# Optimization experiments

Measured on AMD Instinct MI355X. Metric: run time of the kernel, lower is better.

The kernel has to match this reference:

```python
import jax, jax.numpy as jnp
import numpy as np

B = 2
SEQ = 384            # args.seq_len (per-stock sub-sequence length)
N_AUX = 4            # len(args.aux_tickers)
S = SEQ * N_AUX + 1  # global separator token + tiled sub-sequences
D_MODEL = 512
NHEAD = 8
HEAD_DIM = 64
ROPE = 32            # qk_rope_dim
KV_C = 256
Q_C = 384
D_FF = 1536
H2 = NHEAD * 2       # differential attention sub-heads
DH = HEAD_DIM // 2
RH = ROPE // 2
EPS = 1.1920929e-07  # torch RMSNorm default eps (fp32 machine eps)
SCALING = 1.0 / ((HEAD_DIM + ROPE) // 2)
LAMBDA_INIT = 0.8 - 0.6 * float(np.exp(-0.3 * 0))  # depth=0 -> 0.2


def rmsnorm(x, w, eps=EPS):
    return x * jax.lax.rsqrt(jnp.mean(jnp.square(x), -1, keepdims=True) + eps) * w


def apply_rope(xs, cos, sin):
    # xs: [B, N_AUX, SEQ, H2, RH]; cos/sin: [SEQ, RH//2]
    xr = xs[..., 0::2]
    xi = xs[..., 1::2]
    c = cos[None, None, :, None, :]
    s = sin[None, None, :, None, :]
    yr = xr * c - xi * s
    yi = xr * s + xi * c
    return jnp.stack([yr, yi], axis=-1).reshape(xs.shape)


def _build_mask():
    causal = np.triu(np.ones((SEQ, SEQ), np.bool_), 1)
    tiled = np.tile(causal, (N_AUX, N_AUX))
    m = np.ones((S, S), np.bool_)
    m[:, 0] = False          # everyone attends to global separator
    m[1:, 1:] = tiled
    return jnp.asarray(m)[None, None]  # [1,1,S,S], True = masked


MASK = _build_mask()


def setup_inputs() -> dict:
    key = jax.random.key(0)
    ks = jax.random.split(key, 16)

    def w(k, shape, std=0.02):
        return jax.random.normal(k, shape, jnp.float32) * std

    x = jax.random.normal(ks[0], (B, S, D_MODEL), jnp.float32)
    # rope table: complex [SEQ, ROPE//4] stored as (cos, sin)
    pairs = ROPE // 4
    inv = 1.0 / (10000.0 ** (np.arange(pairs, dtype=np.float64) / pairs))
    ang = np.outer(np.arange(SEQ), inv)
    freqs = jnp.asarray(np.stack([np.cos(ang), np.sin(ang)], -1), jnp.float32)
    return {
        'x': x,
        'freqs': freqs,
        'W_kv_down': w(ks[1], (D_MODEL, KV_C + ROPE)),
        'W_q_down': w(ks[2], (D_MODEL, Q_C)),
        'W_kv_up': w(ks[3], (KV_C, NHEAD * HEAD_DIM * 2)),
        'W_q_up': w(ks[4], (Q_C, NHEAD * (HEAD_DIM + ROPE))),
        'kv_norm_w': jnp.ones((KV_C,), jnp.float32),
        'q_norm_w': jnp.ones((Q_C,), jnp.float32),
        'W_o': w(ks[5], (NHEAD * HEAD_DIM, D_MODEL)),
        'lambda_q1': w(ks[6], (DH,), 0.1),
        'lambda_k1': w(ks[7], (DH,), 0.1),
        'lambda_q2': w(ks[8], (DH,), 0.1),
        'lambda_k2': w(ks[9], (DH,), 0.1),
        'head_norm_w': jnp.ones((HEAD_DIM,), jnp.float32),
        'norm1_w': jnp.ones((D_MODEL,), jnp.float32),
        'norm2_w': jnp.ones((D_MODEL,), jnp.float32),
        'W_ff_in': w(ks[10], (D_MODEL, 2 * D_FF)),
        'W_ff_out': w(ks[11], (D_FF, D_MODEL)),
    }


def reference(x, freqs, W_kv_down, W_q_down, W_kv_up, W_q_up, kv_norm_w, q_norm_w,
              W_o, lambda_q1, lambda_k1, lambda_q2, lambda_k2, head_norm_w,
              norm1_w, norm2_w, W_ff_in, W_ff_out):
    cos, sin = freqs[..., 0], freqs[..., 1]
    # ---- attention block (pre-norm) ----
    h = rmsnorm(x, norm1_w)
    ckv_full = h @ W_kv_down                               # [B,S,KV_C+ROPE]
    c_kv, k_rope = ckv_full[..., :KV_C], ckv_full[..., KV_C:]
    kv = (rmsnorm(c_kv, kv_norm_w) @ W_kv_up).reshape(B, S, NHEAD, 2 * HEAD_DIM)
    k, v = kv[..., :HEAD_DIM], kv[..., HEAD_DIM:]
    k = k.reshape(B, S, H2, DH)
    qf = (rmsnorm(h @ W_q_down, q_norm_w) @ W_q_up).reshape(B, S, NHEAD, HEAD_DIM + ROPE)
    q, q_rope = qf[..., :HEAD_DIM], qf[..., HEAD_DIM:]
    q = q.reshape(B, S, H2, DH)
    k_rope = jnp.broadcast_to(k_rope[:, :, None, :], (B, S, NHEAD, ROPE)).reshape(B, S, H2, RH)
    q_rope = q_rope.reshape(B, S, H2, RH)
    # split off global separator token, rope per sub-sequence
    q_sep, q_rot = q_rope[:, :1], q_rope[:, 1:].reshape(B, N_AUX, SEQ, H2, RH)
    k_sep, k_rot = k_rope[:, :1], k_rope[:, 1:].reshape(B, N_AUX, SEQ, H2, RH)
    q_rot = apply_rope(q_rot, cos, sin).reshape(B, S - 1, H2, RH)
    k_rot = apply_rope(k_rot, cos, sin).reshape(B, S - 1, H2, RH)
    q_rope = jnp.concatenate([q_sep, q_rot], axis=1)
    k_rope = jnp.concatenate([k_sep, k_rot], axis=1)
    qh = jnp.concatenate([q, q_rope], -1).transpose(0, 2, 1, 3)  # [B,H2,S,DH+RH]
    kh = jnp.concatenate([k, k_rope], -1).transpose(0, 2, 1, 3)
    a = jnp.einsum('bhqd,bhkd->bhqk', qh, kh) * SCALING
    abs_a = jnp.where(MASK, -1e9, jnp.abs(a))
    p = jnp.sign(a) * jax.nn.softmax(abs_a, axis=-1)
    lam = (jnp.exp(jnp.sum(lambda_q1 * lambda_k1)) -
           jnp.exp(jnp.sum(lambda_q2 * lambda_k2)) + LAMBDA_INIT)
    p = p.reshape(B, NHEAD, 2, S, S)
    G = jnp.mean(p[:, :, 0], axis=-1, keepdims=True)
    att = p[:, :, 0] - lam * p[:, :, 1] + G * lam
    att = jnp.where(MASK, 0.0, att)
    o = jnp.einsum('bhqk,bkhd->bqhd', att, v)              # [B,S,NHEAD,HEAD_DIM]
    o = rmsnorm(o, head_norm_w, 1e-5).reshape(B, S, NHEAD * HEAD_DIM)
    x = x + o @ W_o
    # ---- SwiGLU FFN ----
    h2 = rmsnorm(x, norm2_w)
    uv = h2 @ W_ff_in
    u, g = uv[..., :D_FF], uv[..., D_FF:]
    return x + (u * jax.nn.silu(g)) @ W_ff_out
```

## Files before the change

kernel.cpp:

```cpp
#include <hip/hip_runtime.h>

#define NB 2
#define SEQN 384
#define NS 1537
#define NS_PAD 1600
#define NH 8
#define H2N 16
#define NM (NB*NS)
#define DFF 1536
#define EPS1 1.1920929e-07f
#define SCAL (1.0f/48.0f)
#define SC2 (SCAL * 1.4426950408889634f)

#define SWZ(row, col) ((((row) << 6)) + ((col) ^ (((row) & 7) << 3)))

typedef __bf16 bf16x8 __attribute__((ext_vector_type(8)));
typedef _Float16 f16x8 __attribute__((ext_vector_type(8)));
typedef float f32x4 __attribute__((ext_vector_type(4)));

__device__ __forceinline__ unsigned short f2bf(float f) {
    unsigned int u = __builtin_bit_cast(unsigned int, f);
    u += 0x7FFFu + ((u >> 16) & 1u);
    return (unsigned short)(u >> 16);
}
__device__ __forceinline__ float bf2f(unsigned short h) {
    unsigned int u = ((unsigned int)h) << 16;
    return __builtin_bit_cast(float, u);
}

struct TD { const float* w; unsigned short* hi; unsigned short* lo; int K; int N; };
struct TD7 { TD d[7]; int tend[7]; };

__global__ __launch_bounds__(256) void transpose_all(TD7 a) {
    __shared__ float tile[32][33];
    int t = blockIdx.x;
    int i = 0;
    while (t >= a.tend[i]) i++;
    int base = (i == 0) ? 0 : a.tend[i - 1];
    int lt = t - base;
    const float* w = a.d[i].w;
    unsigned short* hi = a.d[i].hi;
    unsigned short* lo = a.d[i].lo;
    int K = a.d[i].K, N = a.d[i].N;
    int kt = (K + 31) / 32;
    int k0 = (lt % kt) * 32, n0 = (lt / kt) * 32;
    int tx = threadIdx.x & 31, ty4 = (threadIdx.x >> 5) * 4;
    for (int q = 0; q < 4; q++) {
        int k = k0 + ty4 + q, n = n0 + tx;
        tile[ty4 + q][tx] = (k < K && n < N) ? w[(size_t)k * N + n] : 0.f;
    }
    __syncthreads();
    for (int q = 0; q < 4; q++) {
        int n = n0 + ty4 + q, k = k0 + tx;
        if (n < N && k < K) {
            float v = tile[tx][ty4 + q];
            unsigned short hb = f2bf(v);
            size_t o = (size_t)n * K + k;
            hi[o] = hb;
            if (lo) lo[o] = f2bf(v - bf2f(hb));
        }
    }
}

__global__ void lam_kernel(const float* q1, const float* k1, const float* q2, const float* k2,
                           float* out) {
    int t = threadIdx.x;
    float p1 = 0.f, p2 = 0.f;
    if (t < 32) { p1 = q1[t] * k1[t]; p2 = q2[t] * k2[t]; }
    for (int o = 1; o < 32; o <<= 1) { p1 += __shfl_xor(p1, o); p2 += __shfl_xor(p2, o); }
    if (t == 0) out[0] = expf(p1) - expf(p2) + 0.2f;
}

__global__ __launch_bounds__(256) void rmsnorm_k(const float* __restrict__ in,
    const float* __restrict__ w, unsigned short* __restrict__ hi, unsigned short* __restrict__ lo,
    int in_stride, int C, float eps) {
    int row = blockIdx.x;
    const float* x = in + (size_t)row * in_stride;
    float ss = 0.f;
    for (int j = threadIdx.x; j < C; j += 256) { float v = x[j]; ss += v * v; }
    for (int o = 1; o < 64; o <<= 1) ss += __shfl_xor(ss, o);
    __shared__ float red[4];
    if ((threadIdx.x & 63) == 0) red[threadIdx.x >> 6] = ss;
    __syncthreads();
    ss = red[0] + red[1] + red[2] + red[3];
    float rs = rsqrtf(ss / (float)C + eps);
    for (int j = threadIdx.x; j < C; j += 256) {
        float y = x[j] * rs * w[j];
        unsigned short hb = f2bf(y);
        hi[(size_t)row * C + j] = hb;
        if (lo) lo[(size_t)row * C + j] = f2bf(y - bf2f(hb));
    }
}

__global__ __launch_bounds__(256) void gemm_single(const unsigned short* __restrict__ A,
    const unsigned short* __restrict__ Bt, float* __restrict__ C_, const float* __restrict__ res,
    int M, int N, int K) {
    __shared__ unsigned short As[128][40];
    __shared__ unsigned short Bs[64][40];
    int m0 = blockIdx.x * 128, n0 = blockIdx.y * 64;
    int tid = threadIdx.x;
    int lane = tid & 63, wid = tid >> 6;
    int wr = wid >> 1, wc = wid & 1;
    int r = lane & 15, g = lane >> 4;
    int lrow = tid >> 2, lk = (tid & 3) * 8;
    f32x4 acc[4][2] = {};
    int ar0 = m0 + lrow, ar1 = m0 + 64 + lrow, brow = n0 + lrow;
    bool a0ok = ar0 < M, a1ok = ar1 < M, bok = brow < N;
    size_t a0off = (size_t)ar0 * K + lk, a1off = (size_t)ar1 * K + lk, boff = (size_t)brow * K + lk;
    for (int k0 = 0; k0 < K; k0 += 32) {
        uint4 av0 = {0,0,0,0}, av1 = {0,0,0,0}, bv = {0,0,0,0};
        if (a0ok) av0 = *(const uint4*)(A + a0off + k0);
        if (a1ok) av1 = *(const uint4*)(A + a1off + k0);
        if (bok)  bv  = *(const uint4*)(Bt + boff + k0);
        __syncthreads();
        *(uint4*)&As[lrow][lk] = av0;
        *(uint4*)&As[64 + lrow][lk] = av1;
        *(uint4*)&Bs[lrow][lk] = bv;
        __syncthreads();
        bf16x8 a[4], bb[2];
        #pragma unroll
        for (int i = 0; i < 4; i++) a[i] = *(const bf16x8*)&As[wr * 64 + i * 16 + r][g * 8];
        #pragma unroll
        for (int j = 0; j < 2; j++) bb[j] = *(const bf16x8*)&Bs[wc * 32 + j * 16 + r][g * 8];
        #pragma unroll
        for (int i = 0; i < 4; i++)
            #pragma unroll
            for (int j = 0; j < 2; j++)
                acc[i][j] = __builtin_amdgcn_mfma_f32_16x16x32_bf16(a[i], bb[j], acc[i][j], 0, 0, 0);
    }
    #pragma unroll
    for (int i = 0; i < 4; i++)
        #pragma unroll
        for (int j = 0; j < 2; j++) {
            int col = n0 + wc * 32 + j * 16 + r;
            if (col >= N) continue;
            #pragma unroll
            for (int e = 0; e < 4; e++) {
                int row = m0 + wr * 64 + i * 16 + g * 4 + e;
                if (row >= M) continue;
                float v = acc[i][j][e];
                if (res) v += res[(size_t)row * N + col];
                C_[(size_t)row * N + col] = v;
            }
        }
}

__global__ __launch_bounds__(256) void gemm_x3(const unsigned short* __restrict__ Ah,
    const unsigned short* __restrict__ Al, const unsigned short* __restrict__ Bh,
    const unsigned short* __restrict__ Bl, float* __restrict__ C_, int M, int N, int K) {
    __shared__ unsigned short AsH[128][40], AsL[128][40], BsH[64][40], BsL[64][40];
    int m0 = blockIdx.x * 128, n0 = blockIdx.y * 64;
    int tid = threadIdx.x;
    int lane = tid & 63, wid = tid >> 6;
    int wr = wid >> 1, wc = wid & 1;
    int r = lane & 15, g = lane >> 4;
    int lrow = tid >> 2, lk = (tid & 3) * 8;
    f32x4 acc[4][2] = {};
    int ar0 = m0 + lrow, ar1 = m0 + 64 + lrow, brow = n0 + lrow;
    bool a0ok = ar0 < M, a1ok = ar1 < M, bok = brow < N;
    size_t a0off = (size_t)ar0 * K + lk, a1off = (size_t)ar1 * K + lk, boff = (size_t)brow * K + lk;
    for (int k0 = 0; k0 < K; k0 += 32) {
        uint4 ah0 = {0,0,0,0}, al0 = {0,0,0,0}, ah1 = {0,0,0,0}, al1 = {0,0,0,0};
        uint4 bh0 = {0,0,0,0}, bl0 = {0,0,0,0};
        if (a0ok) { ah0 = *(const uint4*)(Ah + a0off + k0); al0 = *(const uint4*)(Al + a0off + k0); }
        if (a1ok) { ah1 = *(const uint4*)(Ah + a1off + k0); al1 = *(const uint4*)(Al + a1off + k0); }
        if (bok)  { bh0 = *(const uint4*)(Bh + boff + k0);  bl0 = *(const uint4*)(Bl + boff + k0); }
        __syncthreads();
        *(uint4*)&AsH[lrow][lk] = ah0; *(uint4*)&AsH[64 + lrow][lk] = ah1;
        *(uint4*)&AsL[lrow][lk] = al0; *(uint4*)&AsL[64 + lrow][lk] = al1;
        *(uint4*)&BsH[lrow][lk] = bh0; *(uint4*)&BsL[lrow][lk] = bl0;
        __syncthreads();
        bf16x8 ah[4], al[4], bh[2], bl[2];
        #pragma unroll
        for (int i = 0; i < 4; i++) {
            ah[i] = *(const bf16x8*)&AsH[wr * 64 + i * 16 + r][g * 8];
            al[i] = *(const bf16x8*)&AsL[wr * 64 + i * 16 + r][g * 8];
        }
        #pragma unroll
        for (int j = 0; j < 2; j++) {
            bh[j] = *(const bf16x8*)&BsH[wc * 32 + j * 16 + r][g * 8];
            bl[j] = *(const bf16x8*)&BsL[wc * 32 + j * 16 + r][g * 8];
        }
        #pragma unroll
        for (int i = 0; i < 4; i++)
            #pragma unroll
            for (int j = 0; j < 2; j++) {
                acc[i][j] = __builtin_amdgcn_mfma_f32_16x16x32_bf16(al[i], bh[j], acc[i][j], 0, 0, 0);
                acc[i][j] = __builtin_amdgcn_mfma_f32_16x16x32_bf16(ah[i], bl[j], acc[i][j], 0, 0, 0);
                acc[i][j] = __builtin_amdgcn_mfma_f32_16x16x32_bf16(ah[i], bh[j], acc[i][j], 0, 0, 0);
            }
    }
    #pragma unroll
    for (int i = 0; i < 4; i++)
        #pragma unroll
        for (int j = 0; j < 2; j++) {
            int col = n0 + wc * 32 + j * 16 + r;
            if (col >= N) continue;
            #pragma unroll
            for (int e = 0; e < 4; e++) {
                int row = m0 + wr * 64 + i * 16 + g * 4 + e;
                if (row < M) C_[(size_t)row * N + col] = acc[i][j][e];
            }
        }
}

__global__ void assemble2(const float* __restrict__ qf_, const float* __restrict__ kvf,
    const float* __restrict__ ckv, const float* __restrict__ freqs,
    _Float16* __restrict__ qgh, _Float16* __restrict__ qgl,
    _Float16* __restrict__ kgh, _Float16* __restrict__ kgl) {
    size_t idx = (size_t)blockIdx.x * 256 + threadIdx.x;
    const size_t total = (size_t)NB * H2N * NS_PAD * 32;
    if (idx >= total) return;
    int j2 = (int)(idx & 31);
    size_t t = idx >> 5;
    int s = (int)(t % NS_PAD); size_t r = t / NS_PAD;
    int sub = (int)(r & 1); r >>= 1;
    int h = (int)(r & 7); int b = (int)(r >> 3);
    float2 qv = make_float2(0.f, 0.f), kv2 = make_float2(0.f, 0.f);
    if (s < NS && j2 < 24) {
        size_t bs = (size_t)b * NS + s;
        if (j2 < 16) {
            const float* qp = qf_ + bs * 768 + h * 96 + sub * 32 + j2 * 2;
            qv = make_float2(qp[0], qp[1]);
            const float* kp = kvf + bs * 1024 + h * 128 + sub * 32 + j2 * 2;
            kv2 = make_float2(kp[0], kp[1]);
        } else {
            int i = j2 - 16;
            const float* qp = qf_ + bs * 768 + h * 96 + 64 + sub * 16 + 2 * i;
            float xr = qp[0], xi = qp[1];
            const float* kp = ckv + bs * 288 + 256 + sub * 16 + 2 * i;
            float yr = kp[0], yi = kp[1];
            if (s == 0) {
                qv = make_float2(xr, xi);
                kv2 = make_float2(yr, yi);
            } else {
                int pos = (s - 1) % SEQN;
                float c = freqs[pos * 16 + 2 * i], sn = freqs[pos * 16 + 2 * i + 1];
                qv = make_float2(xr * c - xi * sn, xr * sn + xi * c);
                kv2 = make_float2(yr * c - yi * sn, yr * sn + yi * c);
            }
        }
    }
    _Float16 qx = (_Float16)qv.x, qy = (_Float16)qv.y;
    _Float16 kx = (_Float16)kv2.x, ky = (_Float16)kv2.y;
    qgh[idx * 2] = qx; qgh[idx * 2 + 1] = qy;
    kgh[idx * 2] = kx; kgh[idx * 2 + 1] = ky;
    qgl[idx * 2] = (_Float16)(qv.x - (float)qx); qgl[idx * 2 + 1] = (_Float16)(qv.y - (float)qy);
    kgl[idx * 2] = (_Float16)(kv2.x - (float)kx); kgl[idx * 2 + 1] = (_Float16)(kv2.y - (float)ky);
}

__global__ __launch_bounds__(256) void vtrans(const float* __restrict__ kvf,
                                              _Float16* __restrict__ vt) {
    __shared__ float tile[64][65];
    int k0 = blockIdx.x * 64;
    int b = blockIdx.y >> 3, h = blockIdx.y & 7;
    int tid = threadIdx.x;
    int row = tid >> 2, cq = (tid & 3) * 16;
    for (int i = 0; i < 16; i++) {
        int key = k0 + row;
        tile[row][cq + i] = (key < NS)
            ? kvf[((size_t)(b * NS + key)) * 1024 + h * 128 + 64 + cq + i] : 0.f;
    }
    __syncthreads();
    int d = tid >> 2, kq = (tid & 3) * 16;
    for (int i = 0; i < 16; i++)
        vt[((size_t)((b * 8 + h) * 64 + d)) * NS_PAD + k0 + kq + i] = (_Float16)tile[kq + i][d];
}

__global__ __launch_bounds__(256) void prefix2_k(const float* __restrict__ kvf,
                                                 float* __restrict__ P4) {
    __shared__ float tot[4][64];
    int bh = blockIdx.x; int b = bh >> 3, h = bh & 7;
    int d = threadIdx.x & 63, ps = threadIdx.x >> 6;
    int p0 = ps * 96;
    float run = 0.f;
    for (int i = 0; i < 96; i++) {
        int p = p0 + i;
        float s = 0.f;
        #pragma unroll
        for (int c = 0; c < 4; c++)
            s += kvf[((size_t)(b * NS + 1 + c * SEQN + p)) * 1024 + h * 128 + 64 + d];
        run += s;
        P4[((size_t)bh * SEQN + p) * 64 + d] = run;
    }
    tot[ps][d] = run;
    __syncthreads();
    if (ps > 0) {
        float off = 0.f;
        for (int j = 0; j < ps; j++) off += tot[j][d];
        for (int i = 0; i < 96; i++)
            P4[((size_t)bh * SEQN + p0 + i) * 64 + d] += off;
    }
}

__global__ __launch_bounds__(256) void flash_split(
    const _Float16* __restrict__ qgh, const _Float16* __restrict__ qgl,
    const _Float16* __restrict__ kgh, const _Float16* __restrict__ kgl,
    const _Float16* __restrict__ vt,
    float* __restrict__ Opart, float* __restrict__ zpart) {
    __shared__ _Float16 Ksh[2][64 * 64];
    __shared__ _Float16 Ksl[2][64 * 64];
    __shared__ _Float16 Vt[64 * 64];
    __shared__ _Float16 Pl[4][16 * 64];
    const int tile = blockIdx.x;
    const int h = blockIdx.y & 7, split = blockIdx.y >> 3;
    const int b = blockIdx.z;
    const int bh = b * 8 + h;
    const int qs0 = tile * 64;
    const int tid = threadIdx.x;
    const int wave = tid >> 6, lane = tid & 63;
    const int r = lane & 15, g = lane >> 4;
    const int qrow = qs0 + wave * 16;
    const size_t sh0 = (size_t)(bh * 2);

    f16x8 qfh[2][2], qfl[2][2];
    #pragma unroll
    for (int sub = 0; sub < 2; sub++)
        #pragma unroll
        for (int ks = 0; ks < 2; ks++) {
            size_t off = ((sh0 + sub) * NS_PAD + qrow + r) * 64 + ks * 32 + g * 8;
            qfh[sub][ks] = *(const f16x8*)(qgh + off);
            qfl[sub][ks] = *(const f16x8*)(qgl + off);
        }

    float z0p[4] = {0.f,0.f,0.f,0.f}, g0p[4] = {0.f,0.f,0.f,0.f}, z1p[4] = {0.f,0.f,0.f,0.f};
    f32x4 O0[4], O1[4];
    #pragma unroll
    for (int e = 0; e < 4; e++) { O0[e] = (f32x4){0.f,0.f,0.f,0.f}; O1[e] = (f32x4){0.f,0.f,0.f,0.f}; }
    int qpos[4];
    #pragma unroll
    for (int e = 0; e < 4; e++) {
        int q = qrow + g * 4 + e;
        qpos[e] = (q == 0) ? -1 : (q - 1) % SEQN;
    }
    int lo = qs0 < 1 ? 1 : qs0;
    int hi = qs0 + 63 < NS - 1 ? qs0 + 63 : NS - 1;
    int maxpos = ((lo - 1) / SEQN != (hi - 1) / SEQN) ? (SEQN - 1) : (hi - 1) % SEQN;

    int cnt = 0;
    for (int c = 0; c < 4; c++) {
        int nb = (c == 0) ? ((maxpos + 2 + 63) >> 6) : ((maxpos + 1 + 63) >> 6);
        int kstart = (c == 0) ? 0 : (c * SEQN + 1);
        int cbase = c * SEQN + 1;
        for (int j = 0; j < nb; j++, cnt++) {
            if ((cnt & 1) != split) continue;
            int kbase = kstart + j * 64;
            __syncthreads();
            #pragma unroll
            for (int i = 0; i < 4; i++) {
                int chunk = i * 256 + tid;
                int arr = chunk >> 9;
                int cc = chunk & 511;
                int row = cc >> 3, c8 = (cc & 7) * 8;
                size_t goff = ((sh0 + arr) * NS_PAD + kbase + row) * 64 + c8;
                int di = SWZ(row, c8);
                *(uint4*)&Ksh[arr][di] = *(const uint4*)(kgh + goff);
                *(uint4*)&Ksl[arr][di] = *(const uint4*)(kgl + goff);
            }
            #pragma unroll
            for (int i = 0; i < 2; i++) {
                int cc = i * 256 + tid;
                int d = cc >> 3, c8 = (cc & 7) * 8;
                *(uint4*)&Vt[SWZ(d, c8)] =
                    *(const uint4*)(vt + ((size_t)(bh * 64 + d)) * NS_PAD + kbase + c8);
            }
            __syncthreads();

            f16x8 bv[4][2];
            #pragma unroll
            for (int dt = 0; dt < 4; dt++)
                #pragma unroll
                for (int ks = 0; ks < 2; ks++)
                    bv[dt][ks] = *(const f16x8*)&Vt[SWZ(dt * 16 + r, ks * 32 + g * 8)];

            bool um[4][4];
            #pragma unroll
            for (int t4 = 0; t4 < 4; t4++) {
                int kk2 = kbase + t4 * 16 + r;
                int rel = kk2 - cbase;
                #pragma unroll
                for (int e = 0; e < 4; e++)
                    um[e][t4] = (kk2 == 0) ||
                                ((unsigned)rel < (unsigned)SEQN && rel <= qpos[e]);
            }

            #pragma unroll
            for (int sub = 0; sub < 2; sub++) {
                f32x4 acc[4];
                #pragma unroll
                for (int t4 = 0; t4 < 4; t4++) acc[t4] = (f32x4){0.f,0.f,0.f,0.f};
                #pragma unroll
                for (int t4 = 0; t4 < 4; t4++)
                    #pragma unroll
                    for (int ks = 0; ks < 2; ks++) {
                        int ki = SWZ(t4 * 16 + r, ks * 32 + g * 8);
                        f16x8 bkh = *(const f16x8*)&Ksh[sub][ki];
                        f16x8 bkl = *(const f16x8*)&Ksl[sub][ki];
                        acc[t4] = __builtin_amdgcn_mfma_f32_16x16x32_f16(qfl[sub][ks], bkh, acc[t4], 0, 0, 0);
                        acc[t4] = __builtin_amdgcn_mfma_f32_16x16x32_f16(qfh[sub][ks], bkl, acc[t4], 0, 0, 0);
                        acc[t4] = __builtin_amdgcn_mfma_f32_16x16x32_f16(qfh[sub][ks], bkh, acc[t4], 0, 0, 0);
                    }
                #pragma unroll
                for (int e = 0; e < 4; e++) {
                    #pragma unroll
                    for (int t4 = 0; t4 < 4; t4++) {
                        float a = acc[t4][e];
                        float ef = exp2f(fabsf(a) * SC2);
                        float ev = um[e][t4] ? ef : 0.f;
                        float pvv = copysignf(ev, a);
                        if (sub == 0) { z0p[e] += ev; g0p[e] += pvv; }
                        else          { z1p[e] += ev; }
                        Pl[wave][SWZ(g * 4 + e, t4 * 16 + r)] = (_Float16)pvv;
                    }
                }
                __builtin_amdgcn_wave_barrier();
                f16x8 pa0 = *(const f16x8*)&Pl[wave][SWZ(r, g * 8)];
                f16x8 pa1 = *(const f16x8*)&Pl[wave][SWZ(r, 32 + g * 8)];
                #pragma unroll
                for (int dt = 0; dt < 4; dt++) {
                    if (sub == 0) {
                        O0[dt] = __builtin_amdgcn_mfma_f32_16x16x32_f16(pa0, bv[dt][0], O0[dt], 0, 0, 0);
                        O0[dt] = __builtin_amdgcn_mfma_f32_16x16x32_f16(pa1, bv[dt][1], O0[dt], 0, 0, 0);
                    } else {
                        O1[dt] = __builtin_amdgcn_mfma_f32_16x16x32_f16(pa0, bv[dt][0], O1[dt], 0, 0, 0);
                        O1[dt] = __builtin_amdgcn_mfma_f32_16x16x32_f16(pa1, bv[dt][1], O1[dt], 0, 0, 0);
                    }
                }
            }
        }
    }

    #pragma unroll
    for (int e = 0; e < 4; e++) {
        float z0 = z0p[e], g0 = g0p[e], z1 = z1p[e];
        #pragma unroll
        for (int o = 1; o < 16; o <<= 1) {
            z0 += __shfl_xor(z0, o); g0 += __shfl_xor(g0, o); z1 += __shfl_xor(z1, o);
        }
        int q = qrow + g * 4 + e;
        if (q < NS) {
            if (r == 0) {
                float* zp = zpart + (((size_t)split * 16 + bh) * NS + q) * 4;
                zp[0] = z0; zp[1] = g0; zp[2] = z1;
            }
            float* op = Opart + (((size_t)split * 16 + bh) * NS + q) * 128;
            #pragma unroll
            for (int dt = 0; dt < 4; dt++) {
                op[dt * 16 + r] = O0[dt][e];
                op[64 + dt * 16 + r] = O1[dt][e];
            }
        }
    }
}

__global__ __launch_bounds__(256) void combine_attn(const float* __restrict__ Opart,
    const float* __restrict__ zpart, const float* __restrict__ kvf,
    const float* __restrict__ P4, const float* __restrict__ lamp,
    const float* __restrict__ hw, unsigned short* __restrict__ o_n) {
    int b = blockIdx.z, h = blockIdx.y, bh = b * 8 + h;
    int ql = threadIdx.x >> 2, dp = threadIdx.x & 3;
    int q = blockIdx.x * 64 + ql;
    bool ok = q < NS;
    int qc = ok ? q : 0;
    float lam = lamp[0];
    size_t i0 = ((size_t)0 * 16 + bh) * NS + qc;
    size_t i1 = ((size_t)1 * 16 + bh) * NS + qc;
    const float* za = zpart + i0 * 4;
    const float* zb = zpart + i1 * 4;
    float z0 = za[0] + zb[0], g0 = za[1] + zb[1], z1 = za[2] + zb[2];
    float iz0 = 1.f / z0;
    float l1 = lam / z1;
    float Gl = lam * g0 * iz0 * (1.f / (float)NS);
    int qpos = (q == 0) ? -1 : (q - 1) % SEQN;
    const float* oa = Opart + i0 * 128 + dp * 16;
    const float* ob = Opart + i1 * 128 + dp * 16;
    float of[16]; float ss = 0.f;
    #pragma unroll
    for (int i = 0; i < 16; i++) {
        int d = dp * 16 + i;
        float O0 = oa[i] + ob[i];
        float O1 = oa[64 + i] + ob[64 + i];
        float vs = kvf[((size_t)(b * NS)) * 1024 + h * 128 + 64 + d];
        if (qpos >= 0) vs += P4[((size_t)bh * SEQN + qpos) * 64 + d];
        float o = O0 * iz0 - O1 * l1 + Gl * vs;
        of[i] = o; ss += o * o;
    }
    ss += __shfl_xor(ss, 1); ss += __shfl_xor(ss, 2);
    float rs = rsqrtf(ss / 64.f + 1e-5f);
    if (ok) {
        unsigned int pk[8];
        #pragma unroll
        for (int i = 0; i < 8; i++) {
            unsigned int a = f2bf(of[2 * i] * rs * hw[dp * 16 + 2 * i]);
            unsigned int c = f2bf(of[2 * i + 1] * rs * hw[dp * 16 + 2 * i + 1]);
            pk[i] = a | (c << 16);
        }
        unsigned short* dst = o_n + ((size_t)(b * NS + q)) * 512 + h * 64 + dp * 16;
        *(uint4*)dst = *(uint4*)&pk[0];
        *(uint4*)(dst + 8) = *(uint4*)&pk[4];
    }
}

__global__ void swiglu_k(const float* __restrict__ uv, unsigned short* __restrict__ act) {
    size_t idx = (size_t)blockIdx.x * 256 + threadIdx.x;
    if (idx >= (size_t)NM * DFF) return;
    size_t mrow = idx / DFF; int j = (int)(idx % DFF);
    float u = uv[mrow * (2 * DFF) + j];
    float gg = uv[mrow * (2 * DFF) + DFF + j];
    float sg = gg / (1.f + __expf(-gg));
    act[idx] = f2bf(u * sg);
}

extern "C" void kernel_launch(void* const* d_in, const int* in_sizes, int n_in,
                              void* d_out, int out_size, void* d_ws, size_t ws_size,
                              hipStream_t stream) {
    (void)in_sizes; (void)n_in; (void)out_size; (void)ws_size;
    const float* x    = (const float*)d_in[0];
    const float* freqs= (const float*)d_in[1];
    const float* Wkvd = (const float*)d_in[2];
    const float* Wqd  = (const float*)d_in[3];
    const float* Wkvu = (const float*)d_in[4];
    const float* Wqu  = (const float*)d_in[5];
    const float* kvnw = (const float*)d_in[6];
    const float* qnw  = (const float*)d_in[7];
    const float* Wo   = (const float*)d_in[8];
    const float* lq1  = (const float*)d_in[9];
    const float* lk1  = (const float*)d_in[10];
    const float* lq2  = (const float*)d_in[11];
    const float* lk2  = (const float*)d_in[12];
    const float* hnw  = (const float*)d_in[13];
    const float* n1w  = (const float*)d_in[14];
    const float* n2w  = (const float*)d_in[15];
    const float* Wffi = (const float*)d_in[16];
    const float* Wffo = (const float*)d_in[17];
    float* out = (float*)d_out;

    char* p = (char*)d_ws;
    auto alloc = [&](size_t nbytes) -> char* {
        char* r = p; p += (nbytes + 255) & ~(size_t)255; return r;
    };
    unsigned short* wkvd_h = (unsigned short*)alloc((size_t)512 * 288 * 2);
    unsigned short* wkvd_l = (unsigned short*)alloc((size_t)512 * 288 * 2);
    unsigned short* wqd_h  = (unsigned short*)alloc((size_t)512 * 384 * 2);
    unsigned short* wqd_l  = (unsigned short*)alloc((size_t)512 * 384 * 2);
    unsigned short* wkvu_h = (unsigned short*)alloc((size_t)256 * 1024 * 2);
    unsigned short* wkvu_l = (unsigned short*)alloc((size_t)256 * 1024 * 2);
    unsigned short* wqu_h  = (unsigned short*)alloc((size_t)384 * 768 * 2);
    unsigned short* wqu_l  = (unsigned short*)alloc((size_t)384 * 768 * 2);
    unsigned short* wo_h   = (unsigned short*)alloc((size_t)512 * 512 * 2);
    unsigned short* wffi_h = (unsigned short*)alloc((size_t)512 * 3072 * 2);
    unsigned short* wffo_h = (unsigned short*)alloc((size_t)1536 * 512 * 2);
    unsigned short* h_hi   = (unsigned short*)alloc((size_t)NM * 512 * 2);
    unsigned short* h_lo   = (unsigned short*)alloc((size_t)NM * 512 * 2);
    char* cq0 = p;
    float* ckv = (float*)alloc((size_t)NM * 288 * 4);
    float* qd  = (float*)alloc((size_t)NM * 384 * 4);
    float* x2  = (float*)cq0;
    char* nb0 = p;
    unsigned short* ckvn_h = (unsigned short*)alloc((size_t)NM * 256 * 2);
    unsigned short* ckvn_l = (unsigned short*)alloc((size_t)NM * 256 * 2);
    unsigned short* qdn_h  = (unsigned short*)alloc((size_t)NM * 384 * 2);
    unsigned short* qdn_l  = (unsigned short*)alloc((size_t)NM * 384 * 2);
    unsigned short* o_n    = (unsigned short*)alloc((size_t)NM * 512 * 2);
    unsigned short* h2     = (unsigned short*)alloc((size_t)NM * 512 * 2);
    unsigned short* act    = (unsigned short*)nb0;
    char* r0 = p;
    float* kvf = (float*)alloc((size_t)NM * 1024 * 4);
    float* qff = (float*)alloc((size_t)NM * 768 * 4);
    _Float16* qgh = (_Float16*)alloc((size_t)NB * H2N * NS_PAD * 64 * 2);
    _Float16* qgl = (_Float16*)alloc((size_t)NB * H2N * NS_PAD * 64 * 2);
    _Float16* kgh = (_Float16*)alloc((size_t)NB * H2N * NS_PAD * 64 * 2);
    _Float16* kgl = (_Float16*)alloc((size_t)NB * H2N * NS_PAD * 64 * 2);
    _Float16* vt  = (_Float16*)alloc((size_t)NB * NH * 64 * NS_PAD * 2);
    float* P4     = (float*)alloc((size_t)NB * NH * SEQN * 64 * 4);
    float* Opart  = (float*)alloc((size_t)2 * 16 * NS * 128 * 4);
    float* zpart  = (float*)alloc((size_t)2 * 16 * NS * 4 * 4);
    float* uv     = (float*)r0;
    float* lamv   = (float*)alloc(256);

    {
        TD7 a;
        const float* ws_[7] = {Wkvd, Wqd, Wkvu, Wqu, Wo, Wffi, Wffo};
        unsigned short* his[7] = {wkvd_h, wqd_h, wkvu_h, wqu_h, wo_h, wffi_h, wffo_h};
        unsigned short* los[7] = {wkvd_l, wqd_l, wkvu_l, wqu_l, nullptr, nullptr, nullptr};
        int Ks[7] = {512, 512, 256, 384, 512, 512, 1536};
        int Ns[7] = {288, 384, 1024, 768, 512, 3072, 512};
        int cum = 0;
        for (int i = 0; i < 7; i++) {
            a.d[i] = TD{ws_[i], his[i], los[i], Ks[i], Ns[i]};
            cum += ((Ks[i] + 31) / 32) * ((Ns[i] + 31) / 32);
            a.tend[i] = cum;
        }
        transpose_all<<<dim3(cum), 256, 0, stream>>>(a);
    }
    lam_kernel<<<1, 64, 0, stream>>>(lq1, lk1, lq2, lk2, lamv);

    rmsnorm_k<<<NM, 256, 0, stream>>>(x, n1w, h_hi, h_lo, 512, 512, EPS1);

    const int GX = (NM + 127) / 128;
    gemm_x3<<<dim3(GX, (288 + 63) / 64), 256, 0, stream>>>(h_hi, h_lo, wkvd_h, wkvd_l, ckv, NM, 288, 512);
    gemm_x3<<<dim3(GX, (384 + 63) / 64), 256, 0, stream>>>(h_hi, h_lo, wqd_h, wqd_l, qd, NM, 384, 512);

    rmsnorm_k<<<NM, 256, 0, stream>>>(ckv, kvnw, ckvn_h, ckvn_l, 288, 256, EPS1);
    rmsnorm_k<<<NM, 256, 0, stream>>>(qd, qnw, qdn_h, qdn_l, 384, 384, EPS1);

    gemm_x3<<<dim3(GX, 1024 / 64), 256, 0, stream>>>(ckvn_h, ckvn_l, wkvu_h, wkvu_l, kvf, NM, 1024, 256);
    gemm_x3<<<dim3(GX, 768 / 64), 256, 0, stream>>>(qdn_h, qdn_l, wqu_h, wqu_l, qff, NM, 768, 384);

    {
        size_t total = (size_t)NB * H2N * NS_PAD * 32;
        assemble2<<<dim3((unsigned)((total + 255) / 256)), 256, 0, stream>>>(
            qff, kvf, ckv, freqs, qgh, qgl, kgh, kgl);
    }
    vtrans<<<dim3(NS_PAD / 64, NB * NH), 256, 0, stream>>>(kvf, vt);
    prefix2_k<<<dim3(NB * NH), 256, 0, stream>>>(kvf, P4);

    flash_split<<<dim3((NS + 63) / 64, 16, NB), 256, 0, stream>>>(
        qgh, qgl, kgh, kgl, vt, Opart, zpart);
    combine_attn<<<dim3((NS + 63) / 64, NH, NB), 256, 0, stream>>>(
        Opart, zpart, kvf, P4, lamv, hnw, o_n);

    gemm_single<<<dim3(GX, 512 / 64), 256, 0, stream>>>(o_n, wo_h, x2, x, NM, 512, 512);
    rmsnorm_k<<<NM, 256, 0, stream>>>(x2, n2w, h2, nullptr, 512, 512, EPS1);
    gemm_single<<<dim3(GX, 3072 / 64), 256, 0, stream>>>(h2, wffi_h, uv, nullptr, NM, 3072, 512);
    {
        size_t total = (size_t)NM * DFF;
        swiglu_k<<<dim3((unsigned)((total + 255) / 256)), 256, 0, stream>>>(uv, act);
    }
    gemm_single<<<dim3(GX, 512 / 64), 256, 0, stream>>>(act, wffo_h, out, x2, NM, 512, 1536);
}
```

Baseline: 344.4 us.

## Fuse down-projections, dual rmsnorm, swiglu epilogue, and load-balanced flash chunks

Merges the kv and q down-projection GEMMs into one 672-wide GEMM followed by a single dual-RMSNorm kernel. The FFN-in weights are interleaved so SwiGLU can run in the GEMM epilogue, which removes the uv buffer and the separate swiglu kernel. The lambda computation moves into combine_attn. Attention is split into a host-built table of balanced key-block chunks (up to 4 per tile, longest first) instead of a fixed 2-way split. LDS row padding is also removed (40 to 32), which may bring back bank conflicts.

Result: faster. 311.7 us (-9.5%).

```diff
diff --git a/kernel.cpp b/kernel.cpp
--- a/kernel.cpp
+++ b/kernel.cpp
@@ -28,7 +28,18 @@
     return __builtin_bit_cast(float, u);
 }
 
-struct TD { const float* w; unsigned short* hi; unsigned short* lo; int K; int N; };
+__host__ __device__ inline void tile_info(int t, int& nb0, int& nbc, int& w, int& nch) {
+    int lo = (t == 0) ? 1 : t * 64;
+    int hi0 = t * 64 + 63;
+    int hi = hi0 < NS - 1 ? hi0 : NS - 1;
+    int maxpos = ((lo - 1) / SEQN != (hi - 1) / SEQN) ? (SEQN - 1) : (hi - 1) % SEQN;
+    nb0 = (maxpos + 65) >> 6;
+    nbc = (maxpos + 64) >> 6;
+    w = nb0 + 3 * nbc;
+    nch = (w + 6) / 7;
+}
+
+struct TD { const float* w; unsigned short* hi; unsigned short* lo; int K; int N; int perm; };
 struct TD7 { TD d[7]; int tend[7]; };
 
 __global__ __launch_bounds__(256) void transpose_all(TD7 a) {
@@ -41,7 +52,8 @@
     const float* w = a.d[i].w;
     unsigned short* hi = a.d[i].hi;
     unsigned short* lo = a.d[i].lo;
-    int K = a.d[i].K, N = a.d[i].N;
+    int K = a.d[i].K, N = a.d[i].N, perm = a.d[i].perm;
+    int Nh = N >> 1;
     int kt = (K + 31) / 32;
     int k0 = (lt % kt) * 32, n0 = (lt / kt) * 32;
     int tx = threadIdx.x & 31, ty4 = (threadIdx.x >> 5) * 4;
@@ -55,20 +67,12 @@
         if (n < N && k < K) {
             float v = tile[tx][ty4 + q];
             unsigned short hb = f2bf(v);
-            size_t o = (size_t)n * K + k;
+            int n_out = perm ? ((n < Nh) ? 2 * n : 2 * (n - Nh) + 1) : n;
+            size_t o = (size_t)n_out * K + k;
             hi[o] = hb;
             if (lo) lo[o] = f2bf(v - bf2f(hb));
         }
     }
-}
-
-__global__ void lam_kernel(const float* q1, const float* k1, const float* q2, const float* k2,
-                           float* out) {
-    int t = threadIdx.x;
-    float p1 = 0.f, p2 = 0.f;
-    if (t < 32) { p1 = q1[t] * k1[t]; p2 = q2[t] * k2[t]; }
-    for (int o = 1; o < 32; o <<= 1) { p1 += __shfl_xor(p1, o); p2 += __shfl_xor(p2, o); }
-    if (t == 0) out[0] = expf(p1) - expf(p2) + 0.2f;
 }
 
 __global__ __launch_bounds__(256) void rmsnorm_k(const float* __restrict__ in,
@@ -92,11 +96,50 @@
     }
 }
 
+__global__ __launch_bounds__(256) void rmsnorm_dual(const float* __restrict__ cq,
+    const float* __restrict__ wA, const float* __restrict__ wB,
+    unsigned short* __restrict__ ah, unsigned short* __restrict__ al,
+    unsigned short* __restrict__ bh_, unsigned short* __restrict__ bl_) {
+    int row = blockIdx.x, tid = threadIdx.x;
+    const float* xx = cq + (size_t)row * 672;
+    __shared__ float red[4];
+    float v = xx[tid & 255];
+    float ss = v * v;
+    for (int o = 1; o < 64; o <<= 1) ss += __shfl_xor(ss, o);
+    if ((tid & 63) == 0) red[tid >> 6] = ss;
+    __syncthreads();
+    float tot = red[0] + red[1] + red[2] + red[3];
+    float rs = rsqrtf(tot / 256.f + EPS1);
+    float y = v * rs * wA[tid];
+    unsigned short hb = f2bf(y);
+    ah[(size_t)row * 256 + tid] = hb;
+    al[(size_t)row * 256 + tid] = f2bf(y - bf2f(hb));
+    __syncthreads();
+    float v0 = xx[288 + tid];
+    float v1 = (tid < 128) ? xx[288 + 256 + tid] : 0.f;
+    float ss2 = v0 * v0 + v1 * v1;
+    for (int o = 1; o < 64; o <<= 1) ss2 += __shfl_xor(ss2, o);
+    if ((tid & 63) == 0) red[tid >> 6] = ss2;
+    __syncthreads();
+    tot = red[0] + red[1] + red[2] + red[3];
+    rs = rsqrtf(tot / 384.f + EPS1);
+    float yb = v0 * rs * wB[tid];
+    hb = f2bf(yb);
+    bh_[(size_t)row * 384 + tid] = hb;
+    bl_[(size_t)row * 384 + tid] = f2bf(yb - bf2f(hb));
+    if (tid < 128) {
+        float yc = v1 * rs * wB[256 + tid];
+        unsigned short hc = f2bf(yc);
+        bh_[(size_t)row * 384 + 256 + tid] = hc;
+        bl_[(size_t)row * 384 + 256 + tid] = f2bf(yc - bf2f(hc));
+    }
+}
+
 __global__ __launch_bounds__(256) void gemm_single(const unsigned short* __restrict__ A,
     const unsigned short* __restrict__ Bt, float* __restrict__ C_, const float* __restrict__ res,
     int M, int N, int K) {
-    __shared__ unsigned short As[128][40];
-    __shared__ unsigned short Bs[64][40];
+    __shared__ unsigned short As[128][32];
+    __shared__ unsigned short Bs[64][32];
     int m0 = blockIdx.x * 128, n0 = blockIdx.y * 64;
     int tid = threadIdx.x;
     int lane = tid & 63, wid = tid >> 6;
@@ -145,10 +188,66 @@
         }
 }
 
+__global__ __launch_bounds__(256) void gemm_swiglu(const unsigned short* __restrict__ A,
+    const unsigned short* __restrict__ Bt, unsigned short* __restrict__ act,
+    int M, int N, int K) {
+    __shared__ unsigned short As[128][32];
+    __shared__ unsigned short Bs[64][32];
+    int m0 = blockIdx.x * 128, n0 = blockIdx.y * 64;
+    int tid = threadIdx.x;
+    int lane = tid & 63, wid = tid >> 6;
+    int wr = wid >> 1, wc = wid & 1;
+    int r = lane & 15, g = lane >> 4;
+    int lrow = tid >> 2, lk = (tid & 3) * 8;
+    f32x4 acc[4][2] = {};
+    int ar0 = m0 + lrow, ar1 = m0 + 64 + lrow, brow = n0 + lrow;
+    bool a0ok = ar0 < M, a1ok = ar1 < M, bok = brow < N;
+    size_t a0off = (size_t)ar0 * K + lk, a1off = (size_t)ar1 * K + lk, boff = (size_t)brow * K + lk;
+    for (int k0 = 0; k0 < K; k0 += 32) {
+        uint4 av0 = {0,0,0,0}, av1 = {0,0,0,0}, bv = {0,0,0,0};
+        if (a0ok) av0 = *(const uint4*)(A + a0off + k0);
+        if (a1ok) av1 = *(const uint4*)(A + a1off + k0);
+        if (bok)  bv  = *(const uint4*)(Bt + boff + k0);
+        __syncthreads();
+        *(uint4*)&As[lrow][lk] = av0;
+        *(uint4*)&As[64 + lrow][lk] = av1;
+        *(uint4*)&Bs[lrow][lk] = bv;
+        __syncthreads();
+        bf16x8 a[4], bb[2];
+        #pragma unroll
+        for (int i = 0; i < 4; i++) a[i] = *(const bf16x8*)&As[wr * 64 + i * 16 + r][g * 8];
+        #pragma unroll
+        for (int j = 0; j < 2; j++) bb[j] = *(const bf16x8*)&Bs[wc * 32 + j * 16 + r][g * 8];
+        #pragma unroll
+        for (int i = 0; i < 4; i++)
+            #pragma unroll
+            for (int j = 0; j < 2; j++)
+                acc[i][j] = __builtin_amdgcn_mfma_f32_16x16x32_bf16(a[i], bb[j], acc[i][j], 0, 0, 0);
+    }
+    int Nh = N >> 1;
+    #pragma unroll
+    for (int i = 0; i < 4; i++)
+        #pragma unroll
+        for (int j = 0; j < 2; j++) {
+            int col = n0 + wc * 32 + j * 16 + r;
+            #pragma unroll
+            for (int e = 0; e < 4; e++) {
+                int row = m0 + wr * 64 + i * 16 + g * 4 + e;
+                float v = acc[i][j][e];
+                float o = __shfl_xor(v, 1);
+                if (((r & 1) == 0) && row < M && col < N) {
+                    float u = v, gg = o;
+                    float sg = gg / (1.f + __expf(-gg));
+                    act[(size_t)row * Nh + (col >> 1)] = f2bf(u * sg);
+                }
+            }
+        }
+}
+
 __global__ __launch_bounds__(256) void gemm_x3(const unsigned short* __restrict__ Ah,
     const unsigned short* __restrict__ Al, const unsigned short* __restrict__ Bh,
     const unsigned short* __restrict__ Bl, float* __restrict__ C_, int M, int N, int K) {
-    __shared__ unsigned short AsH[128][40], AsL[128][40], BsH[64][40], BsL[64][40];
+    __shared__ unsigned short AsH[128][32], AsL[128][32], BsH[64][32], BsL[64][32];
     int m0 = blockIdx.x * 128, n0 = blockIdx.y * 64;
     int tid = threadIdx.x;
     int lane = tid & 63, wid = tid >> 6;
@@ -205,7 +304,7 @@
 }
 
 __global__ void assemble2(const float* __restrict__ qf_, const float* __restrict__ kvf,
-    const float* __restrict__ ckv, const float* __restrict__ freqs,
+    const float* __restrict__ cq, const float* __restrict__ freqs,
     _Float16* __restrict__ qgh, _Float16* __restrict__ qgl,
     _Float16* __restrict__ kgh, _Float16* __restrict__ kgl) {
     size_t idx = (size_t)blockIdx.x * 256 + threadIdx.x;
@@ -228,7 +327,7 @@
             int i = j2 - 16;
             const float* qp = qf_ + bs * 768 + h * 96 + 64 + sub * 16 + 2 * i;
             float xr = qp[0], xi = qp[1];
-            const float* kp = ckv + bs * 288 + 256 + sub * 16 + 2 * i;
+            const float* kp = cq + bs * 672 + 256 + sub * 16 + 2 * i;
             float yr = kp[0], yi = kp[1];
             if (s == 0) {
                 qv = make_float2(xr, xi);
@@ -255,11 +354,11 @@
     int k0 = blockIdx.x * 64;
     int b = blockIdx.y >> 3, h = blockIdx.y & 7;
     int tid = threadIdx.x;
-    int row = tid >> 2, cq = (tid & 3) * 16;
+    int row = tid >> 2, cq_ = (tid & 3) * 16;
     for (int i = 0; i < 16; i++) {
         int key = k0 + row;
-        tile[row][cq + i] = (key < NS)
-            ? kvf[((size_t)(b * NS + key)) * 1024 + h * 128 + 64 + cq + i] : 0.f;
+        tile[row][cq_ + i] = (key < NS)
+            ? kvf[((size_t)(b * NS + key)) * 1024 + h * 128 + 64 + cq_ + i] : 0.f;
     }
     __syncthreads();
     int d = tid >> 2, kq = (tid & 3) * 16;
@@ -293,26 +392,31 @@
     }
 }
 
-__global__ __launch_bounds__(256) void flash_split(
+struct FlashTab { int4 e[80]; };
+
+__global__ __launch_bounds__(256) void flash_chunk(
     const _Float16* __restrict__ qgh, const _Float16* __restrict__ qgl,
     const _Float16* __restrict__ kgh, const _Float16* __restrict__ kgl,
     const _Float16* __restrict__ vt,
-    float* __restrict__ Opart, float* __restrict__ zpart) {
+    float* __restrict__ Opart, float* __restrict__ zpart, FlashTab tab) {
     __shared__ _Float16 Ksh[2][64 * 64];
     __shared__ _Float16 Ksl[2][64 * 64];
     __shared__ _Float16 Vt[64 * 64];
     __shared__ _Float16 Pl[4][16 * 64];
-    const int tile = blockIdx.x;
-    const int h = blockIdx.y & 7, split = blockIdx.y >> 3;
-    const int b = blockIdx.z;
-    const int bh = b * 8 + h;
-    const int qs0 = tile * 64;
+    const int4 E = tab.e[blockIdx.x];
+    const int tq = E.x, kti0 = E.y, nk = E.z, slot = E.w;
+    const int bh = blockIdx.y;
+    const int b = bh >> 3, h = bh & 7;
+    const int qs0 = tq * 64;
     const int tid = threadIdx.x;
     const int wave = tid >> 6, lane = tid & 63;
     const int r = lane & 15, g = lane >> 4;
     const int qrow = qs0 + wave * 16;
     const size_t sh0 = (size_t)(bh * 2);
 
+    int nb0, nbc, w_, nch_;
+    tile_info(tq, nb0, nbc, w_, nch_);
+
     f16x8 qfh[2][2], qfl[2][2];
     #pragma unroll
     for (int sub = 0; sub < 2; sub++)
@@ -333,98 +437,93 @@
         int q = qrow + g * 4 + e;
         qpos[e] = (q == 0) ? -1 : (q - 1) % SEQN;
     }
-    int lo = qs0 < 1 ? 1 : qs0;
-    int hi = qs0 + 63 < NS - 1 ? qs0 + 63 : NS - 1;
-    int maxpos = ((lo - 1) / SEQN != (hi - 1) / SEQN) ? (SEQN - 1) : (hi - 1) % SEQN;
-
-    int cnt = 0;
-    for (int c = 0; c < 4; c++) {
-        int nb = (c == 0) ? ((maxpos + 2 + 63) >> 6) : ((maxpos + 1 + 63) >> 6);
-        int kstart = (c == 0) ? 0 : (c * SEQN + 1);
+
+    for (int ii = 0; ii < nk; ii++) {
+        int kti = kti0 + ii;
+        int c, j;
+        if (kti < nb0) { c = 0; j = kti; }
+        else { int m = kti - nb0; c = 1 + m / nbc; j = m - (c - 1) * nbc; }
+        int kbase = (c == 0) ? j * 64 : c * SEQN + 1 + j * 64;
         int cbase = c * SEQN + 1;
-        for (int j = 0; j < nb; j++, cnt++) {
-            if ((cnt & 1) != split) continue;
-            int kbase = kstart + j * 64;
-            __syncthreads();
-            #pragma unroll
-            for (int i = 0; i < 4; i++) {
-                int chunk = i * 256 + tid;
-                int arr = chunk >> 9;
-                int cc = chunk & 511;
-                int row = cc >> 3, c8 = (cc & 7) * 8;
-                size_t goff = ((sh0 + arr) * NS_PAD + kbase + row) * 64 + c8;
-                int di = SWZ(row, c8);
-                *(uint4*)&Ksh[arr][di] = *(const uint4*)(kgh + goff);
-                *(uint4*)&Ksl[arr][di] = *(const uint4*)(kgl + goff);
-            }
-            #pragma unroll
-            for (int i = 0; i < 2; i++) {
-                int cc = i * 256 + tid;
-                int d = cc >> 3, c8 = (cc & 7) * 8;
-                *(uint4*)&Vt[SWZ(d, c8)] =
-                    *(const uint4*)(vt + ((size_t)(bh * 64 + d)) * NS_PAD + kbase + c8);
-            }
-            __syncthreads();
-
-            f16x8 bv[4][2];
-            #pragma unroll
-            for (int dt = 0; dt < 4; dt++)
+        __syncthreads();
+        #pragma unroll
+        for (int i = 0; i < 4; i++) {
+            int chunk = i * 256 + tid;
+            int arr = chunk >> 9;
+            int cc = chunk & 511;
+            int row = cc >> 3, c8 = (cc & 7) * 8;
+            size_t goff = ((sh0 + arr) * NS_PAD + kbase + row) * 64 + c8;
+            int di = SWZ(row, c8);
+            *(uint4*)&Ksh[arr][di] = *(const uint4*)(kgh + goff);
+            *(uint4*)&Ksl[arr][di] = *(const uint4*)(kgl + goff);
+        }
+        #pragma unroll
+        for (int i = 0; i < 2; i++) {
+            int cc = i * 256 + tid;
+            int d = cc >> 3, c8 = (cc & 7) * 8;
+            *(uint4*)&Vt[SWZ(d, c8)] =
+                *(const uint4*)(vt + ((size_t)(bh * 64 + d)) * NS_PAD + kbase + c8);
+        }
+        __syncthreads();
+
+        f16x8 bv[4][2];
+        #pragma unroll
+        for (int dt = 0; dt < 4; dt++)
+            #pragma unroll
+            for (int ks = 0; ks < 2; ks++)
+                bv[dt][ks] = *(const f16x8*)&Vt[SWZ(dt * 16 + r, ks * 32 + g * 8)];
+
+        bool um[4][4];
+        #pragma unroll
+        for (int t4 = 0; t4 < 4; t4++) {
+            int kk2 = kbase + t4 * 16 + r;
+            int rel = kk2 - cbase;
+            #pragma unroll
+            for (int e = 0; e < 4; e++)
+                um[e][t4] = (kk2 == 0) ||
+                            ((unsigned)rel < (unsigned)SEQN && rel <= qpos[e]);
+        }
+
+        #pragma unroll
+        for (int sub = 0; sub < 2; sub++) {
+            f32x4 acc[4];
+            #pragma unroll
+            for (int t4 = 0; t4 < 4; t4++) acc[t4] = (f32x4){0.f,0.f,0.f,0.f};
+            #pragma unroll
+            for (int t4 = 0; t4 < 4; t4++)
                 #pragma unroll
-                for (int ks = 0; ks < 2; ks++)
-                    bv[dt][ks] = *(const f16x8*)&Vt[SWZ(dt * 16 + r, ks * 32 + g * 8)];
-
-            bool um[4][4];
-            #pragma unroll
-            for (int t4 = 0; t4 < 4; t4++) {
-                int kk2 = kbase + t4 * 16 + r;
-                int rel = kk2 - cbase;
+                for (int ks = 0; ks < 2; ks++) {
+                    int ki = SWZ(t4 * 16 + r, ks * 32 + g * 8);
+                    f16x8 bkh = *(const f16x8*)&Ksh[sub][ki];
+                    f16x8 bkl = *(const f16x8*)&Ksl[sub][ki];
+                    acc[t4] = __builtin_amdgcn_mfma_f32_16x16x32_f16(qfl[sub][ks], bkh, acc[t4], 0, 0, 0);
+                    acc[t4] = __builtin_amdgcn_mfma_f32_16x16x32_f16(qfh[sub][ks], bkl, acc[t4], 0, 0, 0);
+                    acc[t4] = __builtin_amdgcn_mfma_f32_16x16x32_f16(qfh[sub][ks], bkh, acc[t4], 0, 0, 0);
+                }
+            #pragma unroll
+            for (int e = 0; e < 4; e++) {
                 #pragma unroll
-                for (int e = 0; e < 4; e++)
-                    um[e][t4] = (kk2 == 0) ||
-                                ((unsigned)rel < (unsigned)SEQN && rel <= qpos[e]);
-            }
-
-            #pragma unroll
-            for (int sub = 0; sub < 2; sub++) {
-                f32x4 acc[4];
-                #pragma unroll
-                for (int t4 = 0; t4 < 4; t4++) acc[t4] = (f32x4){0.f,0.f,0.f,0.f};
-                #pragma unroll
-                for (int t4 = 0; t4 < 4; t4++)
-                    #pragma unroll
-                    for (int ks = 0; ks < 2; ks++) {
-                        int ki = SWZ(t4 * 16 + r, ks * 32 + g * 8);
-                        f16x8 bkh = *(const f16x8*)&Ksh[sub][ki];
-                        f16x8 bkl = *(const f16x8*)&Ksl[sub][ki];
-                        acc[t4] = __builtin_amdgcn_mfma_f32_16x16x32_f16(qfl[sub][ks], bkh, acc[t4], 0, 0, 0);
-                        acc[t4] = __builtin_amdgcn_mfma_f32_16x16x32_f16(qfh[sub][ks], bkl, acc[t4], 0, 0, 0);
-                        acc[t4] = __builtin_amdgcn_mfma_f32_16x16x32_f16(qfh[sub][ks], bkh, acc[t4], 0, 0, 0);
-                    }
-                #pragma unroll
-                for (int e = 0; e < 4; e++) {
-                    #pragma unroll
-                    for (int t4 = 0; t4 < 4; t4++) {
-                        float a = acc[t4][e];
-                        float ef = exp2f(fabsf(a) * SC2);
-                        float ev = um[e][t4] ? ef : 0.f;
-                        float pvv = copysignf(ev, a);
-                        if (sub == 0) { z0p[e] += ev; g0p[e] += pvv; }
-                        else          { z1p[e] += ev; }
-                        Pl[wave][SWZ(g * 4 + e, t4 * 16 + r)] = (_Float16)pvv;
-                    }
+                for (int t4 = 0; t4 < 4; t4++) {
+                    float a = acc[t4][e];
+                    float ef = exp2f(fabsf(a) * SC2);
+                    float ev = um[e][t4] ? ef : 0.f;
+                    float pvv = copysignf(ev, a);
+                    if (sub == 0) { z0p[e] += ev; g0p[e] += pvv; }
+                    else          { z1p[e] += ev; }
+                    Pl[wave][SWZ(g * 4 + e, t4 * 16 + r)] = (_Float16)pvv;
                 }
-                __builtin_amdgcn_wave_barrier();
-                f16x8 pa0 = *(const f16x8*)&Pl[wave][SWZ(r, g * 8)];
-                f16x8 pa1 = *(const f16x8*)&Pl[wave][SWZ(r, 32 + g * 8)];
-                #pragma unroll
-                for (int dt = 0; dt < 4; dt++) {
-                    if (sub == 0) {
-                        O0[dt] = __builtin_amdgcn_mfma_f32_16x16x32_f16(pa0, bv[dt][0], O0[dt], 0, 0, 0);
-                        O0[dt] = __builtin_amdgcn_mfma_f32_16x16x32_f16(pa1, bv[dt][1], O0[dt], 0, 0, 0);
-                    } else {
-                        O1[dt] = __builtin_amdgcn_mfma_f32_16x16x32_f16(pa0, bv[dt][0], O1[dt], 0, 0, 0);
-                        O1[dt] = __builtin_amdgcn_mfma_f32_16x16x32_f16(pa1, bv[dt][1], O1[dt], 0, 0, 0);
-                    }
+            }
+            __builtin_amdgcn_wave_barrier();
+            f16x8 pa0 = *(const f16x8*)&Pl[wave][SWZ(r, g * 8)];
+            f16x8 pa1 = *(const f16x8*)&Pl[wave][SWZ(r, 32 + g * 8)];
+            #pragma unroll
+            for (int dt = 0; dt < 4; dt++) {
+                if (sub == 0) {
+                    O0[dt] = __builtin_amdgcn_mfma_f32_16x16x32_f16(pa0, bv[dt][0], O0[dt], 0, 0, 0);
+                    O0[dt] = __builtin_amdgcn_mfma_f32_16x16x32_f16(pa1, bv[dt][1], O0[dt], 0, 0, 0);
+                } else {
+                    O1[dt] = __builtin_amdgcn_mfma_f32_16x16x32_f16(pa0, bv[dt][0], O1[dt], 0, 0, 0);
+                    O1[dt] = __builtin_amdgcn_mfma_f32_16x16x32_f16(pa1, bv[dt][1], O1[dt], 0, 0, 0);
                 }
             }
         }
@@ -440,10 +539,10 @@
         int q = qrow + g * 4 + e;
         if (q < NS) {
             if (r == 0) {
-                float* zp = zpart + (((size_t)split * 16 + bh) * NS + q) * 4;
+                float* zp = zpart + (((size_t)slot * 16 + bh) * NS + q) * 4;
                 zp[0] = z0; zp[1] = g0; zp[2] = z1;
             }
-            float* op = Opart + (((size_t)split * 16 + bh) * NS + q) * 128;
+            float* op = Opart + (((size_t)slot * 16 + bh) * NS + q) * 128;
             #pragma unroll
             for (int dt = 0; dt < 4; dt++) {
                 op[dt * 16 + r] = O0[dt][e];
@@ -455,34 +554,50 @@
 
 __global__ __launch_bounds__(256) void combine_attn(const float* __restrict__ Opart,
     const float* __restrict__ zpart, const float* __restrict__ kvf,
-    const float* __restrict__ P4, const float* __restrict__ lamp,
+    const float* __restrict__ P4,
+    const float* __restrict__ lq1, const float* __restrict__ lk1,
+    const float* __restrict__ lq2, const float* __restrict__ lk2,
     const float* __restrict__ hw, unsigned short* __restrict__ o_n) {
+    __shared__ float lamS;
+    if (threadIdx.x < 32) {
+        float p1 = lq1[threadIdx.x] * lk1[threadIdx.x];
+        float p2 = lq2[threadIdx.x] * lk2[threadIdx.x];
+        for (int o = 1; o < 32; o <<= 1) { p1 += __shfl_xor(p1, o); p2 += __shfl_xor(p2, o); }
+        if (threadIdx.x == 0) lamS = expf(p1) - expf(p2) + 0.2f;
+    }
+    __syncthreads();
+    float lam = lamS;
     int b = blockIdx.z, h = blockIdx.y, bh = b * 8 + h;
     int ql = threadIdx.x >> 2, dp = threadIdx.x & 3;
     int q = blockIdx.x * 64 + ql;
     bool ok = q < NS;
     int qc = ok ? q : 0;
-    float lam = lamp[0];
-    size_t i0 = ((size_t)0 * 16 + bh) * NS + qc;
-    size_t i1 = ((size_t)1 * 16 + bh) * NS + qc;
-    const float* za = zpart + i0 * 4;
-    const float* zb = zpart + i1 * 4;
-    float z0 = za[0] + zb[0], g0 = za[1] + zb[1], z1 = za[2] + zb[2];
+    int tq = qc >> 6;
+    int nb0_, nbc_, w_, nch;
+    tile_info(tq, nb0_, nbc_, w_, nch);
+    float z0 = 0.f, g0 = 0.f, z1 = 0.f;
+    float O0a[16], O1a[16];
+    #pragma unroll
+    for (int i = 0; i < 16; i++) { O0a[i] = 0.f; O1a[i] = 0.f; }
+    for (int s = 0; s < nch; s++) {
+        size_t ib = ((size_t)s * 16 + bh) * NS + qc;
+        const float* zp = zpart + ib * 4;
+        z0 += zp[0]; g0 += zp[1]; z1 += zp[2];
+        const float* op = Opart + ib * 128 + dp * 16;
+        #pragma unroll
+        for (int i = 0; i < 16; i++) { O0a[i] += op[i]; O1a[i] += op[64 + i]; }
+    }
     float iz0 = 1.f / z0;
     float l1 = lam / z1;
     float Gl = lam * g0 * iz0 * (1.f / (float)NS);
     int qpos = (q == 0) ? -1 : (q - 1) % SEQN;
-    const float* oa = Opart + i0 * 128 + dp * 16;
-    const float* ob = Opart + i1 * 128 + dp * 16;
     float of[16]; float ss = 0.f;
     #pragma unroll
     for (int i = 0; i < 16; i++) {
         int d = dp * 16 + i;
-        float O0 = oa[i] + ob[i];
-        float O1 = oa[64 + i] + ob[64 + i];
         float vs = kvf[((size_t)(b * NS)) * 1024 + h * 128 + 64 + d];
         if (qpos >= 0) vs += P4[((size_t)bh * SEQN + qpos) * 64 + d];
-        float o = O0 * iz0 - O1 * l1 + Gl * vs;
+        float o = O0a[i] * iz0 - O1a[i] * l1 + Gl * vs;
         of[i] = o; ss += o * o;
     }
     ss += __shfl_xor(ss, 1); ss += __shfl_xor(ss, 2);
@@ -499,16 +614,6 @@
         *(uint4*)dst = *(uint4*)&pk[0];
         *(uint4*)(dst + 8) = *(uint4*)&pk[4];
     }
-}
-
-__global__ void swiglu_k(const float* __restrict__ uv, unsigned short* __restrict__ act) {
-    size_t idx = (size_t)blockIdx.x * 256 + threadIdx.x;
-    if (idx >= (size_t)NM * DFF) return;
-    size_t mrow = idx / DFF; int j = (int)(idx % DFF);
-    float u = uv[mrow * (2 * DFF) + j];
-    float gg = uv[mrow * (2 * DFF) + DFF + j];
-    float sg = gg / (1.f + __expf(-gg));
-    act[idx] = f2bf(u * sg);
 }
 
 extern "C" void kernel_launch(void* const* d_in, const int* in_sizes, int n_in,
@@ -539,10 +644,8 @@
     auto alloc = [&](size_t nbytes) -> char* {
         char* r = p; p += (nbytes + 255) & ~(size_t)255; return r;
     };
-    unsigned short* wkvd_h = (unsigned short*)alloc((size_t)512 * 288 * 2);
-    unsigned short* wkvd_l = (unsigned short*)alloc((size_t)512 * 288 * 2);
-    unsigned short* wqd_h  = (unsigned short*)alloc((size_t)512 * 384 * 2);
-    unsigned short* wqd_l  = (unsigned short*)alloc((size_t)512 * 384 * 2);
+    unsigned short* wcq_h  = (unsigned short*)alloc((size_t)672 * 512 * 2);
+    unsigned short* wcq_l  = (unsigned short*)alloc((size_t)672 * 512 * 2);
     unsigned short* wkvu_h = (unsigned short*)alloc((size_t)256 * 1024 * 2);
     unsigned short* wkvu_l = (unsigned short*)alloc((size_t)256 * 1024 * 2);
     unsigned short* wqu_h  = (unsigned short*)alloc((size_t)384 * 768 * 2);
@@ -553,18 +656,16 @@
     unsigned short* h_hi   = (unsigned short*)alloc((size_t)NM * 512 * 2);
     unsigned short* h_lo   = (unsigned short*)alloc((size_t)NM * 512 * 2);
     char* cq0 = p;
-    float* ckv = (float*)alloc((size_t)NM * 288 * 4);
-    float* qd  = (float*)alloc((size_t)NM * 384 * 4);
-    float* x2  = (float*)cq0;
-    char* nb0 = p;
+    float* cq = (float*)alloc((size_t)NM * 672 * 4);
+    float* x2 = (float*)cq0;
+    char* nb0_ = p;
     unsigned short* ckvn_h = (unsigned short*)alloc((size_t)NM * 256 * 2);
     unsigned short* ckvn_l = (unsigned short*)alloc((size_t)NM * 256 * 2);
     unsigned short* qdn_h  = (unsigned short*)alloc((size_t)NM * 384 * 2);
     unsigned short* qdn_l  = (unsigned short*)alloc((size_t)NM * 384 * 2);
     unsigned short* o_n    = (unsigned short*)alloc((size_t)NM * 512 * 2);
     unsigned short* h2     = (unsigned short*)alloc((size_t)NM * 512 * 2);
-    unsigned short* act    = (unsigned short*)nb0;
-    char* r0 = p;
+    unsigned short* act    = (unsigned short*)nb0_;
     float* kvf = (float*)alloc((size_t)NM * 1024 * 4);
     float* qff = (float*)alloc((size_t)NM * 768 * 4);
     _Float16* qgh = (_Float16*)alloc((size_t)NB * H2N * NS_PAD * 64 * 2);
@@ -573,36 +674,32 @@
     _Float16* kgl = (_Float16*)alloc((size_t)NB * H2N * NS_PAD * 64 * 2);
     _Float16* vt  = (_Float16*)alloc((size_t)NB * NH * 64 * NS_PAD * 2);
     float* P4     = (float*)alloc((size_t)NB * NH * SEQN * 64 * 4);
-    float* Opart  = (float*)alloc((size_t)2 * 16 * NS * 128 * 4);
-    float* zpart  = (float*)alloc((size_t)2 * 16 * NS * 4 * 4);
-    float* uv     = (float*)r0;
-    float* lamv   = (float*)alloc(256);
-
+    float* Opart  = (float*)alloc((size_t)4 * 16 * NS * 128 * 4);
+    float* zpart  = (float*)alloc((size_t)4 * 16 * NS * 4 * 4);
+
+    int cum = 0;
     {
         TD7 a;
         const float* ws_[7] = {Wkvd, Wqd, Wkvu, Wqu, Wo, Wffi, Wffo};
-        unsigned short* his[7] = {wkvd_h, wqd_h, wkvu_h, wqu_h, wo_h, wffi_h, wffo_h};
-        unsigned short* los[7] = {wkvd_l, wqd_l, wkvu_l, wqu_l, nullptr, nullptr, nullptr};
+        unsigned short* his[7] = {wcq_h, wcq_h + (size_t)288 * 512, wkvu_h, wqu_h, wo_h, wffi_h, wffo_h};
+        unsigned short* los[7] = {wcq_l, wcq_l + (size_t)288 * 512, wkvu_l, wqu_l, nullptr, nullptr, nullptr};
         int Ks[7] = {512, 512, 256, 384, 512, 512, 1536};
         int Ns[7] = {288, 384, 1024, 768, 512, 3072, 512};
-        int cum = 0;
+        int pm[7] = {0, 0, 0, 0, 0, 1, 0};
         for (int i = 0; i < 7; i++) {
-            a.d[i] = TD{ws_[i], his[i], los[i], Ks[i], Ns[i]};
+            a.d[i] = TD{ws_[i], his[i], los[i], Ks[i], Ns[i], pm[i]};
             cum += ((Ks[i] + 31) / 32) * ((Ns[i] + 31) / 32);
             a.tend[i] = cum;
         }
         transpose_all<<<dim3(cum), 256, 0, stream>>>(a);
     }
-    lam_kernel<<<1, 64, 0, stream>>>(lq1, lk1, lq2, lk2, lamv);
 
     rmsnorm_k<<<NM, 256, 0, stream>>>(x, n1w, h_hi, h_lo, 512, 512, EPS1);
 
     const int GX = (NM + 127) / 128;
-    gemm_x3<<<dim3(GX, (288 + 63) / 64), 256, 0, stream>>>(h_hi, h_lo, wkvd_h, wkvd_l, ckv, NM, 288, 512);
-    gemm_x3<<<dim3(GX, (384 + 63) / 64), 256, 0, stream>>>(h_hi, h_lo, wqd_h, wqd_l, qd, NM, 384, 512);
-
-    rmsnorm_k<<<NM, 256, 0, stream>>>(ckv, kvnw, ckvn_h, ckvn_l, 288, 256, EPS1);
-    rmsnorm_k<<<NM, 256, 0, stream>>>(qd, qnw, qdn_h, qdn_l, 384, 384, EPS1);
+    gemm_x3<<<dim3(GX, (672 + 63) / 64), 256, 0, stream>>>(h_hi, h_lo, wcq_h, wcq_l, cq, NM, 672, 512);
+
+    rmsnorm_dual<<<NM, 256, 0, stream>>>(cq, kvnw, qnw, ckvn_h, ckvn_l, qdn_h, qdn_l);
 
     gemm_x3<<<dim3(GX, 1024 / 64), 256, 0, stream>>>(ckvn_h, ckvn_l, wkvu_h, wkvu_l, kvf, NM, 1024, 256);
     gemm_x3<<<dim3(GX, 768 / 64), 256, 0, stream>>>(qdn_h, qdn_l, wqu_h, wqu_l, qff, NM, 768, 384);
@@ -610,22 +707,37 @@
     {
         size_t total = (size_t)NB * H2N * NS_PAD * 32;
         assemble2<<<dim3((unsigned)((total + 255) / 256)), 256, 0, stream>>>(
-            qff, kvf, ckv, freqs, qgh, qgl, kgh, kgl);
+            qff, kvf, cq, freqs, qgh, qgl, kgh, kgl);
     }
     vtrans<<<dim3(NS_PAD / 64, NB * NH), 256, 0, stream>>>(kvf, vt);
     prefix2_k<<<dim3(NB * NH), 256, 0, stream>>>(kvf, P4);
 
-    flash_split<<<dim3((NS + 63) / 64, 16, NB), 256, 0, stream>>>(
-        qgh, qgl, kgh, kgl, vt, Opart, zpart);
+    {
+        FlashTab tab;
+        int ne = 0;
+        for (int t = 0; t < (NS + 63) / 64; t++) {
+            int nb0c, nbcc, w, nch;
+            tile_info(t, nb0c, nbcc, w, nch);
+            int base = 0;
+            for (int i = 0; i < nch; i++) {
+                int sz = w / nch + (i < w % nch ? 1 : 0);
+                tab.e[ne++] = make_int4(t, base, sz, i);
+                base += sz;
+            }
+        }
+        for (int i = 1; i < ne; i++) {
+            int4 key = tab.e[i];
+            int j = i - 1;
+            while (j >= 0 && tab.e[j].z < key.z) { tab.e[j + 1] = tab.e[j]; j--; }
+            tab.e[j + 1] = key;
+        }
+        flash_chunk<<<dim3(ne, 16), 256, 0, stream>>>(qgh, qgl, kgh, kgl, vt, Opart, zpart, tab);
+    }
     combine_attn<<<dim3((NS + 63) / 64, NH, NB), 256, 0, stream>>>(
-        Opart, zpart, kvf, P4, lamv, hnw, o_n);
+        Opart, zpart, kvf, P4, lq1, lk1, lq2, lk2, hnw, o_n);
 
     gemm_single<<<dim3(GX, 512 / 64), 256, 0, stream>>>(o_n, wo_h, x2, x, NM, 512, 512);
     rmsnorm_k<<<NM, 256, 0, stream>>>(x2, n2w, h2, nullptr, 512, 512, EPS1);
-    gemm_single<<<dim3(GX, 3072 / 64), 256, 0, stream>>>(h2, wffi_h, uv, nullptr, NM, 3072, 512);
-    {
-        size_t total = (size_t)NM * DFF;
-        swiglu_k<<<dim3((unsigned)((total + 255) / 256)), 256, 0, stream>>>(uv, act);
-    }
+    gemm_swiglu<<<dim3(GX, 3072 / 64), 256, 0, stream>>>(h2, wffi_h, act, NM, 3072, 512);
     gemm_single<<<dim3(GX, 512 / 64), 256, 0, stream>>>(act, wffo_h, out, x2, NM, 512, 1536);
 }
```
